# Performance work log

Measured on AMD Instinct MI355X. Metric: run time of the kernel, lower is better.

The kernel has to match this reference:

```python
import jax, jax.numpy as jnp
import numpy as np
import math

B, S, D, H = 2, 2048, 1024, 16
HD = D // H  # 64 head dim
DFF = 4 * D
ROPE_BASE = 10000.0
EPS = 1e-5


def setup_inputs() -> dict:
    key = jax.random.key(0)
    ks = jax.random.split(key, 16)
    w = lambda k, shp: jax.random.normal(k, shp, jnp.float32) * 0.02
    return {
        "x": jax.random.normal(ks[0], (B, S, D), jnp.float32),
        "Wq": w(ks[1], (D, D)), "bq": jnp.zeros((D,), jnp.float32),
        "Wk": w(ks[2], (D, D)), "bk": jnp.zeros((D,), jnp.float32),
        "Wv": w(ks[3], (D, D)), "bv": jnp.zeros((D,), jnp.float32),
        "Wo": w(ks[4], (D, D)), "bo": jnp.zeros((D,), jnp.float32),
        "W1": w(ks[5], (D, DFF)), "b1": jnp.zeros((DFF,), jnp.float32),
        "W2": w(ks[6], (DFF, D)), "b2": jnp.zeros((D,), jnp.float32),
        "g_pre": jnp.ones((D,), jnp.float32), "be_pre": jnp.zeros((D,), jnp.float32),
        "g_post": jnp.ones((D,), jnp.float32), "be_post": jnp.zeros((D,), jnp.float32),
    }


def _layernorm(x, g, b):
    mu = jnp.mean(x, axis=-1, keepdims=True)
    var = jnp.mean(jnp.square(x - mu), axis=-1, keepdims=True)
    return (x - mu) * jax.lax.rsqrt(var + EPS) * g + b


def _rope(q, k):
    # q,k: [B,H,S,HD]; standard rotary embedding on head dim
    half = HD // 2
    inv_freq = 1.0 / (ROPE_BASE ** (jnp.arange(0, HD, 2, dtype=jnp.float32) / HD))  # [half]
    pos = jnp.arange(S, dtype=jnp.float32)
    freqs = pos[:, None] * inv_freq[None, :]           # [S, half]
    emb = jnp.concatenate([freqs, freqs], axis=-1)      # [S, HD]
    cos = jnp.cos(emb)[None, None]                      # [1,1,S,HD]
    sin = jnp.sin(emb)[None, None]

    def rot_half(t):
        return jnp.concatenate([-t[..., half:], t[..., :half]], axis=-1)

    return q * cos + rot_half(q) * sin, k * cos + rot_half(k) * sin


def reference(x, Wq, bq, Wk, bk, Wv, bv, Wo, bo, W1, b1, W2, b2,
              g_pre, be_pre, g_post, be_post):
    residual = x
    xn = _layernorm(x, g_pre, be_pre)

    def split_heads(t):  # [B,S,D] -> [B,H,S,HD]
        return t.reshape(B, S, H, HD).transpose(0, 2, 1, 3)

    q = split_heads(xn @ Wq + bq)
    k = split_heads(xn @ Wk + bk)
    v = split_heads(xn @ Wv + bv)
    q, k = _rope(q, k)

    scores = jnp.einsum("bhqd,bhkd->bhqk", q, k) / math.sqrt(HD)
    attn = jax.nn.softmax(scores, axis=-1)
    # NOTE: original applies causal mask AFTER softmax with fill -1e9 (no renorm)
    causal = jnp.tril(jnp.ones((S, S), jnp.float32))
    attn = jnp.where(causal == 0, jnp.float32(-1e9), attn)

    out = jnp.einsum("bhqk,bhkd->bhqd", attn, v)        # [B,H,S,HD]
    out = out.transpose(0, 2, 1, 3).reshape(B, S, D)
    out = out @ Wo + bo
    x = residual + out

    residual = x
    xn = _layernorm(x, g_post, be_post)
    ff = jax.nn.relu(xn @ W1 + b1) @ W2 + b2
    return residual + ff
```

## Files before the change

kernel.cpp:

```cpp
#include <hip/hip_runtime.h>
#include <stdint.h>

#define B_ 2
#define S_ 2048
#define D_ 1024
#define H_ 16
#define HD_ 64
#define DFF_ 4096
#define M_ 4096
#define QKV_STR 3072

typedef float           f4_t  __attribute__((ext_vector_type(4)));
typedef unsigned int    ui4_t __attribute__((ext_vector_type(4)));
typedef unsigned int    ui2_t __attribute__((ext_vector_type(2)));
typedef unsigned short  us4_t __attribute__((ext_vector_type(4)));
typedef unsigned short  us8_t __attribute__((ext_vector_type(8)));
typedef __bf16          bf8_t __attribute__((ext_vector_type(8)));

__device__ __forceinline__ float b2f(unsigned short u) {
    union { unsigned int u; float f; } v; v.u = ((unsigned int)u) << 16; return v.f;
}
__device__ __forceinline__ unsigned short f2b(float f) {
    union { float f; unsigned int u; } v; v.f = f;
    unsigned int u = v.u + 0x7fffu + ((v.u >> 16) & 1u);
    return (unsigned short)(u >> 16);
}
__device__ __forceinline__ unsigned cvt_pk_bf16(float lo, float hi) {
    unsigned r;
    asm("v_cvt_pk_bf16_f32 %0, %1, %2" : "=v"(r) : "v"(lo), "v"(hi));
    return r;
}
__device__ __forceinline__ void gll16(const unsigned short* g, unsigned short* l) {
    __builtin_amdgcn_global_load_lds((const __attribute__((address_space(1))) unsigned int*)g,
                                     (__attribute__((address_space(3))) unsigned int*)l,
                                     16, 0, 0);
}

__global__ __launch_bounds__(256) void k_prep(const float* __restrict__ Wq, const float* __restrict__ Wk,
                                              const float* __restrict__ Wv, const float* __restrict__ Wo,
                                              const float* __restrict__ W1, const float* __restrict__ W2,
                                              const float* __restrict__ bq, const float* __restrict__ bk,
                                              const float* __restrict__ bv,
                                              unsigned short* __restrict__ WqkvT, unsigned short* __restrict__ WoT,
                                              unsigned short* __restrict__ W1T, unsigned short* __restrict__ W2T,
                                              float* __restrict__ bqkv, float* __restrict__ tab) {
    const int j = blockIdx.x;
    if (j < 12288) {
        const float* src; unsigned short* dst; int R, C, jj;
        if (j < 3072)      { const int r = j >> 10; src = r == 0 ? Wq : (r == 1 ? Wk : Wv);
                             dst = WqkvT + (size_t)r * 1024 * 1024; R = 1024; C = 1024; jj = j & 1023; }
        else if (j < 4096) { src = Wo; dst = WoT; R = 1024; C = 1024; jj = j - 3072; }
        else if (j < 8192) { src = W1; dst = W1T; R = 1024; C = 4096; jj = j - 4096; }
        else               { src = W2; dst = W2T; R = 4096; C = 1024; jj = j - 8192; }
        const int ntx = C >> 5;
        const int bc = (jj % ntx) * 32, br = (jj / ntx) * 32;
        __shared__ float tile[32][33];
        const int tx = threadIdx.x & 31, ty = threadIdx.x >> 5;
#pragma unroll
        for (int i = ty; i < 32; i += 8)
            tile[i][tx] = src[(size_t)(br + i) * C + bc + tx];
        __syncthreads();
#pragma unroll
        for (int i = ty; i < 32; i += 8)
            dst[(size_t)(bc + i) * R + br + tx] = f2b(tile[tx][i]);
    } else if (j < 12300) {
        const int t = (j - 12288) * 256 + threadIdx.x;
        if (t < 1024) bqkv[t] = bq[t];
        else if (t < 2048) bqkv[t] = bk[t - 1024];
        else if (t < 3072) bqkv[t] = bv[t - 2048];
    } else {
        const int base = (j - 12300) * 256 + threadIdx.x;
#pragma unroll
        for (int e = 0; e < 32; e++) {
            const int idx = base + e * 2048;
            const int s = idx >> 5, i = idx & 31;
            const float freq = exp2f(-(float)i * 0.4152410118609203f);
            float sn, cs;
            sincosf((float)s * freq, &sn, &cs);
            tab[s * 64 + i] = cs;
            tab[s * 64 + 32 + i] = sn;
        }
    }
}

__global__ __launch_bounds__(256) void k_layernorm(const float* __restrict__ x,
                                                   const float* __restrict__ g,
                                                   const float* __restrict__ be,
                                                   unsigned short* __restrict__ out) {
    const int row = blockIdx.x;
    const int t = threadIdx.x;
    const float* xr = x + (size_t)row * D_;
    f4_t v = *(const f4_t*)&xr[t * 4];
    float s = v[0] + v[1] + v[2] + v[3];
#pragma unroll
    for (int o = 32; o >= 1; o >>= 1) s += __shfl_down(s, o);
    __shared__ float red[4];
    const int w = t >> 6, lane = t & 63;
    if (lane == 0) red[w] = s;
    __syncthreads();
    const float mean = (red[0] + red[1] + red[2] + red[3]) * (1.f / D_);
    f4_t d;
#pragma unroll
    for (int c = 0; c < 4; c++) d[c] = v[c] - mean;
    float ss = d[0]*d[0] + d[1]*d[1] + d[2]*d[2] + d[3]*d[3];
#pragma unroll
    for (int o = 32; o >= 1; o >>= 1) ss += __shfl_down(ss, o);
    __syncthreads();
    if (lane == 0) red[w] = ss;
    __syncthreads();
    const float var = (red[0] + red[1] + red[2] + red[3]) * (1.f / D_);
    const float rstd = rsqrtf(var + 1e-5f);
    f4_t gv = *(const f4_t*)&g[t * 4];
    f4_t bv = *(const f4_t*)&be[t * 4];
    us4_t o4;
#pragma unroll
    for (int c = 0; c < 4; c++) o4[c] = f2b(d[c] * rstd * gv[c] + bv[c]);
    *(us4_t*)&out[(size_t)row * D_ + t * 4] = o4;
}

#define VMW(n) asm volatile("s_waitcnt vmcnt(" #n ")" ::: "memory")
#define BAR()  __builtin_amdgcn_s_barrier()

template<int RELU, int BF16OUT, int RESID, int ROPE, int SPLIT>
__global__ __launch_bounds__(256) void k_gemm_bt(const unsigned short* __restrict__ A,
                                                 const unsigned short* __restrict__ Bt,
                                                 const float* __restrict__ bias,
                                                 const float* __restrict__ resid,
                                                 void* __restrict__ Cout,
                                                 const float* __restrict__ tab,
                                                 int M, int N, int K, int ldk, int nbx) {
    __shared__ __align__(16) unsigned short As0[128 * 32];
    __shared__ __align__(16) unsigned short Bs0[128 * 32];
    __shared__ __align__(16) unsigned short As1[128 * 32];
    __shared__ __align__(16) unsigned short Bs1[128 * 32];
    const int tid = threadIdx.x;
    const int cpx = gridDim.x >> 3;
    int nid = (blockIdx.x & 7) * cpx + (blockIdx.x >> 3);
    int half = 0;
    if (SPLIT) { half = nid >> 8; nid &= 255; A += 2048 * half; Bt += 2048 * half; }
    const int m0 = (nid / nbx) * 128, n0 = (nid % nbx) * 128;
    const int w = tid >> 6, lane = tid & 63;
    const int wr = w >> 1, wc = w & 1;
    const int lr = lane & 15, lg = lane >> 4;

    f4_t acc[4][4] = {};

    const int r1 = tid >> 2, q1 = tid & 3;
    const unsigned short* pA1 = A + (size_t)(m0 + r1) * ldk + q1 * 8;
    const unsigned short* pA2 = pA1 + (size_t)64 * ldk;
    const unsigned short* pB1 = Bt + (size_t)(n0 + r1) * ldk + q1 * 8;
    const unsigned short* pB2 = pB1 + (size_t)64 * ldk;
    const int wofs = w * 512;

#define STAGE(AS, BS, kk) do {                 \
        gll16(pA1 + (kk), (AS) + wofs);        \
        gll16(pA2 + (kk), (AS) + 2048 + wofs); \
        gll16(pB1 + (kk), (BS) + wofs);        \
        gll16(pB2 + (kk), (BS) + 2048 + wofs); } while (0)

#define COMPUTE(AS, BS) do {                                                     \
        bf8_t af[4], bfr[4];                                                     \
        _Pragma("unroll")                                                        \
        for (int f = 0; f < 4; f++) {                                            \
            af[f]  = *(const bf8_t*)&(AS)[(wr * 64 + f * 16 + lr) * 32 + lg * 8];\
            bfr[f] = *(const bf8_t*)&(BS)[(wc * 64 + f * 16 + lr) * 32 + lg * 8];\
        }                                                                        \
        _Pragma("unroll")                                                        \
        for (int mf = 0; mf < 4; mf++)                                           \
            _Pragma("unroll")                                                    \
            for (int nf = 0; nf < 4; nf++)                                       \
                acc[mf][nf] = __builtin_amdgcn_mfma_f32_16x16x32_bf16(           \
                    af[mf], bfr[nf], acc[mf][nf], 0, 0, 0); } while (0)

    STAGE(As0, Bs0, 0);
    for (int k0 = 0; k0 + 64 < K; k0 += 64) {
        STAGE(As1, Bs1, k0 + 32);
        VMW(4); BAR();
        COMPUTE(As0, Bs0);
        BAR();
        STAGE(As0, Bs0, k0 + 64);
        VMW(4); BAR();
        COMPUTE(As1, Bs1);
        BAR();
    }
    STAGE(As1, Bs1, K - 32);
    VMW(4); BAR();
    COMPUTE(As0, Bs0);
    VMW(0); BAR();
    COMPUTE(As1, Bs1);
#undef STAGE
#undef COMPUTE

    if (SPLIT) {
        unsigned short* outp = (unsigned short*)Cout + (size_t)half * ((size_t)M * N);
#pragma unroll
        for (int mf = 0; mf < 4; mf++)
#pragma unroll
            for (int nf = 0; nf < 4; nf++) {
                const int n = n0 + wc * 64 + nf * 16 + lr;
#pragma unroll
                for (int j = 0; j < 4; j++) {
                    const int m = m0 + wr * 64 + mf * 16 + lg * 4 + j;
                    outp[(size_t)m * N + n] = f2b(acc[mf][nf][j]);
                }
            }
        return;
    }
    if (ROPE) {
#pragma unroll
        for (int mf = 0; mf < 4; mf++)
#pragma unroll
            for (int nf = 0; nf < 4; nf++) {
                const float bv = bias[n0 + wc * 64 + nf * 16 + lr];
#pragma unroll
                for (int j = 0; j < 4; j++) acc[mf][nf][j] += bv;
            }
        if (n0 < 2048) {
#pragma unroll
            for (int mf = 0; mf < 4; mf++)
#pragma unroll
                for (int j = 0; j < 4; j++) {
                    const int srow = (m0 + wr * 64 + mf * 16 + lg * 4 + j) & 2047;
                    const float* tr = tab + srow * 64;
#pragma unroll
                    for (int t = 0; t < 2; t++) {
                        const float cs = tr[t * 16 + lr];
                        const float sn = tr[32 + t * 16 + lr];
                        const float lo = acc[mf][t][j], hi = acc[mf][t + 2][j];
                        acc[mf][t][j]     = lo * cs - hi * sn;
                        acc[mf][t + 2][j] = hi * cs + lo * sn;
                    }
                }
        }
        unsigned short* outp = (unsigned short*)Cout;
#pragma unroll
        for (int mf = 0; mf < 4; mf++)
#pragma unroll
            for (int nf = 0; nf < 4; nf++) {
                const int n = n0 + wc * 64 + nf * 16 + lr;
#pragma unroll
                for (int j = 0; j < 4; j++) {
                    const int m = m0 + wr * 64 + mf * 16 + lg * 4 + j;
                    outp[(size_t)m * N + n] = f2b(acc[mf][nf][j]);
                }
            }
        return;
    }
#pragma unroll
    for (int mf = 0; mf < 4; mf++) {
#pragma unroll
        for (int nf = 0; nf < 4; nf++) {
            const int n = n0 + wc * 64 + nf * 16 + lr;
            const float bv = bias[n];
#pragma unroll
            for (int j = 0; j < 4; j++) {
                const int m = m0 + wr * 64 + mf * 16 + lg * 4 + j;
                float val = acc[mf][nf][j] + bv;
                if (RESID) val += resid[(size_t)m * N + n];
                if (RELU) val = fmaxf(val, 0.f);
                if (BF16OUT) ((unsigned short*)Cout)[(size_t)m * N + n] = f2b(val);
                else         ((float*)Cout)[(size_t)m * N + n] = val;
            }
        }
    }
}

template<int RELU, int BF16OUT, int RESID>
__global__ __launch_bounds__(256) void k_gemm64(const unsigned short* __restrict__ A,
                                                const unsigned short* __restrict__ Bt,
                                                const float* __restrict__ bias,
                                                const float* __restrict__ resid,
                                                void* __restrict__ Cout,
                                                int M, int N, int K, int ldk, int nbx) {
    __shared__ __align__(16) unsigned short As0[64 * 32];
    __shared__ __align__(16) unsigned short Bs0[128 * 32];
    __shared__ __align__(16) unsigned short As1[64 * 32];
    __shared__ __align__(16) unsigned short Bs1[128 * 32];
    const int tid = threadIdx.x;
    const int cpx = gridDim.x >> 3;
    const int nid = (blockIdx.x & 7) * cpx + (blockIdx.x >> 3);
    const int m0 = (nid / nbx) * 64, n0 = (nid % nbx) * 128;
    const int w = tid >> 6, lane = tid & 63;
    const int wr = w >> 1, wc = w & 1;
    const int lr = lane & 15, lg = lane >> 4;

    f4_t acc[2][4] = {};

    const int r1 = tid >> 2, q1 = tid & 3;
    const unsigned short* pA1 = A + (size_t)(m0 + r1) * ldk + q1 * 8;
    const unsigned short* pB1 = Bt + (size_t)(n0 + r1) * ldk + q1 * 8;
    const unsigned short* pB2 = pB1 + (size_t)64 * ldk;
    const int wofs = w * 512;

#define STAGE(AS, BS, kk) do {                 \
        gll16(pA1 + (kk), (AS) + wofs);        \
        gll16(pB1 + (kk), (BS) + wofs);        \
        gll16(pB2 + (kk), (BS) + 2048 + wofs); } while (0)

#define COMPUTE(AS, BS) do {                                                     \
        bf8_t af[2], bfr[4];                                                     \
        _Pragma("unroll")                                                        \
        for (int f = 0; f < 2; f++)                                              \
            af[f] = *(const bf8_t*)&(AS)[(wr * 32 + f * 16 + lr) * 32 + lg * 8]; \
        _Pragma("unroll")                                                        \
        for (int f = 0; f < 4; f++)                                              \
            bfr[f] = *(const bf8_t*)&(BS)[(wc * 64 + f * 16 + lr) * 32 + lg * 8];\
        _Pragma("unroll")                                                        \
        for (int mf = 0; mf < 2; mf++)                                           \
            _Pragma("unroll")                                                    \
            for (int nf = 0; nf < 4; nf++)                                       \
                acc[mf][nf] = __builtin_amdgcn_mfma_f32_16x16x32_bf16(           \
                    af[mf], bfr[nf], acc[mf][nf], 0, 0, 0); } while (0)

    STAGE(As0, Bs0, 0);
    for (int k0 = 0; k0 + 64 < K; k0 += 64) {
        STAGE(As1, Bs1, k0 + 32);
        VMW(3); BAR();
        COMPUTE(As0, Bs0);
        BAR();
        STAGE(As0, Bs0, k0 + 64);
        VMW(3); BAR();
        COMPUTE(As1, Bs1);
        BAR();
    }
    STAGE(As1, Bs1, K - 32);
    VMW(3); BAR();
    COMPUTE(As0, Bs0);
    VMW(0); BAR();
    COMPUTE(As1, Bs1);
#undef STAGE
#undef COMPUTE

#pragma unroll
    for (int mf = 0; mf < 2; mf++) {
#pragma unroll
        for (int nf = 0; nf < 4; nf++) {
            const int n = n0 + wc * 64 + nf * 16 + lr;
            const float bv = bias[n];
#pragma unroll
            for (int j = 0; j < 4; j++) {
                const int m = m0 + wr * 32 + mf * 16 + lg * 4 + j;
                float val = acc[mf][nf][j] + bv;
                if (RESID) val += resid[(size_t)m * N + n];
                if (RELU) val = fmaxf(val, 0.f);
                if (BF16OUT) ((unsigned short*)Cout)[(size_t)m * N + n] = f2b(val);
                else         ((float*)Cout)[(size_t)m * N + n] = val;
            }
        }
    }
}

__global__ __launch_bounds__(256) void k_comb(const unsigned short* __restrict__ p,
                                              const float* __restrict__ x2,
                                              const float* __restrict__ b2,
                                              float* __restrict__ out) {
    const size_t idx = ((size_t)blockIdx.x * 256 + threadIdx.x) * 8;
    us8_t a = *(const us8_t*)(p + idx);
    us8_t b = *(const us8_t*)(p + (size_t)M_ * D_ + idx);
    const int n = (int)(idx & (D_ - 1));
    f4_t x0 = *(const f4_t*)(x2 + idx), x1 = *(const f4_t*)(x2 + idx + 4);
    f4_t b0 = *(const f4_t*)(b2 + n),  b1 = *(const f4_t*)(b2 + n + 4);
    f4_t o0, o1;
#pragma unroll
    for (int c = 0; c < 4; c++) {
        o0[c] = x0[c] + b0[c] + b2f(a[c]) + b2f(b[c]);
        o1[c] = x1[c] + b1[c] + b2f(a[4 + c]) + b2f(b[4 + c]);
    }
    *(f4_t*)(out + idx) = o0;
    *(f4_t*)(out + idx + 4) = o1;
}

__global__ __launch_bounds__(256) void k_vchunksum(const unsigned short* __restrict__ V,
                                                   float* __restrict__ sums) {
    const int blk = blockIdx.x;
    const int bh = blk >> 5, c = blk & 31;
    const int b = bh >> 4, h = bh & 15;
    const int d = threadIdx.x & 63, r4 = threadIdx.x >> 6;
    const unsigned short* base = V + ((size_t)(b * S_ + c * 64 + r4 * 16)) * QKV_STR + h * HD_ + d;
    float s = 0.f;
#pragma unroll
    for (int r = 0; r < 16; r++) s += b2f(base[(size_t)r * QKV_STR]);
    __shared__ float red[4][64];
    red[r4][d] = s;
    __syncthreads();
    if (r4 == 0) sums[(size_t)blk * 64 + d] = red[0][d] + red[1][d] + red[2][d] + red[3][d];
}

__global__ __launch_bounds__(64) void k_vscan(const float* __restrict__ sums,
                                              float* __restrict__ pre) {
    const int bh = blockIdx.x, d = threadIdx.x;
    float cum = 0.f;
    for (int c = 0; c < 32; c++) {
        pre[((size_t)bh * 33 + c) * 64 + d] = cum;
        cum += sums[((size_t)bh * 32 + c) * 64 + d];
    }
    pre[((size_t)bh * 33 + 32) * 64 + d] = cum;
}

#define KS_STRIDE 72

__global__ __launch_bounds__(256) void k_attn_mfma(const unsigned short* __restrict__ QKV,
                                                   const float* __restrict__ vpre,
                                                   unsigned short* __restrict__ Out) {
    __shared__ __align__(16) unsigned short Ks[2][64 * KS_STRIDE];
    __shared__ __align__(16) unsigned short Vt[2][64 * 64];
    __shared__ __align__(16) unsigned short Ps[4][2][16 * KS_STRIDE];

    const int id = blockIdx.x;
    const int wg = (id & 7) * 64 + (id >> 3);
    const int qblk = 15 - (wg & 15);
    const int bh = wg >> 4;
    const int b = bh >> 4, h = bh & 15;
    const int q0 = qblk * 128;
    const int tid = threadIdx.x;
    const int wq = tid >> 6;
    const int lane = tid & 63;
    const int lr = lane & 15, lg = lane >> 4;

    const unsigned short* Qp = QKV;
    const unsigned short* Kp = QKV + 1024;
    const unsigned short* Vp = QKV + 2048;

    const int kcd = 2 * qblk + (wq >> 1);
    const int lastV = 2 * qblk + 1;
    int qb[2];
    qb[0] = (wq & 1) * 32 + lr;
    qb[1] = qb[0] + 16;

    bf8_t qfrag[2][2];
#pragma unroll
    for (int t = 0; t < 2; t++) {
        const float qs = 0.125f * 1.44269504f;
        const size_t qbase = ((size_t)(b * S_ + q0 + wq * 32 + t * 16 + lr)) * QKV_STR + h * HD_;
#pragma unroll
        for (int ks = 0; ks < 2; ks++) {
            us8_t raw = *(const us8_t*)(Qp + qbase + ks * 32 + lg * 8);
            ui4_t p;
#pragma unroll
            for (int e = 0; e < 4; e++)
                p[e] = cvt_pk_bf16(b2f(raw[e * 2]) * qs, b2f(raw[e * 2 + 1]) * qs);
            union { ui4_t u; bf8_t b; } c; c.u = p;
            qfrag[t][ks] = c.b;
        }
    }

    const int row0 = tid >> 3, g = tid & 7;
    const int row1 = row0 + 32;
    const int r7 = row0 & 7;
    const int wv = tid >> 6;
    const unsigned short* pK0 = Kp + ((size_t)(b * S_ + row0)) * QKV_STR + h * HD_ + g * 8;
    const unsigned short* pK1 = Kp + ((size_t)(b * S_ + row1)) * QKV_STR + h * HD_ + g * 8;
    const unsigned short* pV0 = Vp + ((size_t)(b * S_ + row0)) * QKV_STR + h * HD_ + g * 8;
    const unsigned short* pV1 = Vp + ((size_t)(b * S_ + row1)) * QKV_STR + h * HD_ + g * 8;
    const int sw0 = (wv ^ g) << 3;
    const int sw1 = ((wv + 4) ^ g) << 3;

    float l_run[2] = {0.f, 0.f};
    f4_t acc_o[2][4] = {};
    f4_t acc_pre[2][4] = {};

    ui4_t ck0 = *(const ui4_t*)pK0;
    ui4_t ck1 = *(const ui4_t*)pK1;
    ui4_t cv0 = *(const ui4_t*)pV0;
    ui4_t cv1 = *(const ui4_t*)pV1;
    *(ui4_t*)&Ks[0][row0 * KS_STRIDE + g * 8] = ck0;
    *(ui4_t*)&Ks[0][row1 * KS_STRIDE + g * 8] = ck1;
    {
        const unsigned short* v0 = (const unsigned short*)&cv0;
        const unsigned short* v1 = (const unsigned short*)&cv1;
#pragma unroll
        for (int e = 0; e < 8; e++) {
            const int d = g * 8 + e;
            Vt[0][d * 64 + sw0 + r7] = v0[e];
            Vt[0][d * 64 + sw1 + r7] = v1[e];
        }
    }
    {
        const size_t koff = (size_t)64 * QKV_STR;
        ck0 = *(const ui4_t*)(pK0 + koff);
        ck1 = *(const ui4_t*)(pK1 + koff);
        cv0 = *(const ui4_t*)(pV0 + koff);
        cv1 = *(const ui4_t*)(pV1 + koff);
    }
    __syncthreads();

#define VSLOT(dd, ks) ((((ks) * 4 + lg) ^ (((dd) * 2 + (lr >> 3)) & 7)) << 3)

    for (int kc = 0; kc < 32; kc++) {
        const int cur = kc & 1;
        const unsigned short* Kc = Ks[cur];
        const unsigned short* Vc = Vt[cur];

        f4_t s4[2][4] = {};
        __builtin_amdgcn_s_setprio(1);
#pragma unroll
        for (int ks = 0; ks < 2; ks++) {
#pragma unroll
            for (int kk = 0; kk < 4; kk++) {
                bf8_t kfr = *(const bf8_t*)&Kc[(kk * 16 + lr) * KS_STRIDE + ks * 32 + lg * 8];
                s4[0][kk] = __builtin_amdgcn_mfma_f32_16x16x32_bf16(kfr, qfrag[0][ks], s4[0][kk], 0, 0, 0);
                s4[1][kk] = __builtin_amdgcn_mfma_f32_16x16x32_bf16(kfr, qfrag[1][ks], s4[1][kk], 0, 0, 0);
            }
        }
        __builtin_amdgcn_s_setprio(0);

        if (kc < 31) {
            unsigned short* Kn = Ks[cur ^ 1];
            *(ui4_t*)&Kn[row0 * KS_STRIDE + g * 8] = ck0;
            *(ui4_t*)&Kn[row1 * KS_STRIDE + g * 8] = ck1;
            if (kc + 1 <= lastV) {
                unsigned short* Vn = Vt[cur ^ 1];
                const unsigned short* v0 = (const unsigned short*)&cv0;
                const unsigned short* v1 = (const unsigned short*)&cv1;
#pragma unroll
                for (int e = 0; e < 8; e++) {
                    const int d = g * 8 + e;
                    Vn[d * 64 + sw0 + r7] = v0[e];
                    Vn[d * 64 + sw1 + r7] = v1[e];
                }
            }
        }
        if (kc < 30) {
            const size_t koff = (size_t)(kc + 2) * 64 * QKV_STR;
            ck0 = *(const ui4_t*)(pK0 + koff);
            ck1 = *(const ui4_t*)(pK1 + koff);
            if (kc + 2 <= lastV) {
                cv0 = *(const ui4_t*)(pV0 + koff);
                cv1 = *(const ui4_t*)(pV1 + koff);
            }
        }

#pragma unroll
        for (int t = 0; t < 2; t++) {
            float cs = 0.f;
#pragma unroll
            for (int kk = 0; kk < 4; kk++)
#pragma unroll
                for (int j = 0; j < 4; j++) {
                    const float p = __builtin_amdgcn_exp2f(s4[t][kk][j]);
                    s4[t][kk][j] = p;
                    cs += p;
                }
            cs += __shfl_xor(cs, 16);
            cs += __shfl_xor(cs, 32);
            l_run[t] += cs;
        }

        if (kc <= kcd) {
#pragma unroll
            for (int t = 0; t < 2; t++) {
                unsigned short* Pw = Ps[wq][t];
#pragma unroll
                for (int kk = 0; kk < 4; kk++) {
                    const int kb = kk * 16 + lg * 4;
                    ui2_t wd;
                    if (kc == kcd) {
                        wd[0] = cvt_pk_bf16(kb + 0 <= qb[t] ? s4[t][kk][0] : 0.f,
                                            kb + 1 <= qb[t] ? s4[t][kk][1] : 0.f);
                        wd[1] = cvt_pk_bf16(kb + 2 <= qb[t] ? s4[t][kk][2] : 0.f,
                                            kb + 3 <= qb[t] ? s4[t][kk][3] : 0.f);
                    } else {
                        wd[0] = cvt_pk_bf16(s4[t][kk][0], s4[t][kk][1]);
                        wd[1] = cvt_pk_bf16(s4[t][kk][2], s4[t][kk][3]);
                    }
                    *(ui2_t*)&Pw[lr * KS_STRIDE + kk * 16 + lg * 4] = wd;
                }
            }
            __builtin_amdgcn_s_setprio(1);
#pragma unroll
            for (int ks = 0; ks < 2; ks++) {
                bf8_t pf0 = *(const bf8_t*)&Ps[wq][0][lr * KS_STRIDE + ks * 32 + lg * 8];
                bf8_t pf1 = *(const bf8_t*)&Ps[wq][1][lr * KS_STRIDE + ks * 32 + lg * 8];
#pragma unroll
                for (int dd = 0; dd < 4; dd++) {
                    bf8_t vf = *(const bf8_t*)&Vc[(dd * 16 + lr) * 64 + VSLOT(dd, ks)];
                    acc_o[0][dd] = __builtin_amdgcn_mfma_f32_16x16x32_bf16(vf, pf0, acc_o[0][dd], 0, 0, 0);
                    acc_o[1][dd] = __builtin_amdgcn_mfma_f32_16x16x32_bf16(vf, pf1, acc_o[1][dd], 0, 0, 0);
                }
            }
            __builtin_amdgcn_s_setprio(0);

            if (kc == kcd) {
#pragma unroll
                for (int t = 0; t < 2; t++) {
                    unsigned short* Pw = Ps[wq][t];
#pragma unroll
                    for (int kk = 0; kk < 4; kk++) {
                        const int kb = kk * 16 + lg * 4;
                        ui2_t wd;
                        wd[0] = (kb + 0 <= qb[t] ? 0x3f80u : 0u) | ((kb + 1 <= qb[t] ? 0x3f80u : 0u) << 16);
                        wd[1] = (kb + 2 <= qb[t] ? 0x3f80u : 0u) | ((kb + 3 <= qb[t] ? 0x3f80u : 0u) << 16);
                        *(ui2_t*)&Pw[lr * KS_STRIDE + kk * 16 + lg * 4] = wd;
                    }
                }
#pragma unroll
                for (int ks = 0; ks < 2; ks++) {
                    bf8_t pf0 = *(const bf8_t*)&Ps[wq][0][lr * KS_STRIDE + ks * 32 + lg * 8];
                    bf8_t pf1 = *(const bf8_t*)&Ps[wq][1][lr * KS_STRIDE + ks * 32 + lg * 8];
#pragma unroll
                    for (int dd = 0; dd < 4; dd++) {
                        bf8_t vf = *(const bf8_t*)&Vc[(dd * 16 + lr) * 64 + VSLOT(dd, ks)];
                        acc_pre[0][dd] = __builtin_amdgcn_mfma_f32_16x16x32_bf16(vf, pf0, acc_pre[0][dd], 0, 0, 0);
                        acc_pre[1][dd] = __builtin_amdgcn_mfma_f32_16x16x32_bf16(vf, pf1, acc_pre[1][dd], 0, 0, 0);
                    }
                }
            }
        }
        __syncthreads();
    }
#undef VSLOT

    const float* Cq = vpre + ((size_t)bh * 33 + kcd) * 64;
    const float* Ct = vpre + ((size_t)bh * 33 + 32) * 64;
#pragma unroll
    for (int t = 0; t < 2; t++) {
        const float inv_l = 1.f / l_run[t];
        const size_t obase = ((size_t)(b * S_ + q0 + wq * 32 + t * 16 + lr)) * D_ + h * HD_;
#pragma unroll
        for (int dd = 0; dd < 4; dd++) {
            const f4_t tq4 = *(const f4_t*)&Cq[dd * 16 + lg * 4];
            const f4_t tt4 = *(const f4_t*)&Ct[dd * 16 + lg * 4];
            float v[4];
#pragma unroll
            for (int j = 0; j < 4; j++)
                v[j] = acc_o[t][dd][j] * inv_l - 1e9f * (tt4[j] - tq4[j] - acc_pre[t][dd][j]);
            ui2_t wd;
            wd[0] = cvt_pk_bf16(v[0], v[1]);
            wd[1] = cvt_pk_bf16(v[2], v[3]);
            *(ui2_t*)&Out[obase + dd * 16 + lg * 4] = wd;
        }
    }
}

extern "C" void kernel_launch(void* const* d_in, const int* in_sizes, int n_in,
                              void* d_out, int out_size, void* d_ws, size_t ws_size,
                              hipStream_t stream) {
    const float* x     = (const float*)d_in[0];
    const float* Wq    = (const float*)d_in[1];  const float* bq = (const float*)d_in[2];
    const float* Wk    = (const float*)d_in[3];  const float* bk = (const float*)d_in[4];
    const float* Wv    = (const float*)d_in[5];  const float* bv = (const float*)d_in[6];
    const float* Wo    = (const float*)d_in[7];  const float* bo = (const float*)d_in[8];
    const float* W1    = (const float*)d_in[9];  const float* b1 = (const float*)d_in[10];
    const float* W2    = (const float*)d_in[11]; const float* b2 = (const float*)d_in[12];
    const float* gpre  = (const float*)d_in[13]; const float* bepre  = (const float*)d_in[14];
    const float* gpost = (const float*)d_in[15]; const float* bepost = (const float*)d_in[16];

    char* ws = (char*)d_ws;
    const size_t MB = 1024 * 1024;
    unsigned short* psplit = (unsigned short*)(ws + 0 * MB);
    unsigned short* WqkvT = (unsigned short*)(ws + 0 * MB);
    unsigned short* WoT   = (unsigned short*)(ws + 6 * MB);
    unsigned short* W1T   = (unsigned short*)(ws + 8 * MB);
    unsigned short* W2T   = (unsigned short*)(ws + 16 * MB);
    unsigned short* xn    = (unsigned short*)(ws + 24 * MB);
    unsigned short* x2n   = (unsigned short*)(ws + 24 * MB);
    unsigned short* QKV   = (unsigned short*)(ws + 32 * MB);
    unsigned short* h1    = (unsigned short*)(ws + 32 * MB);
    unsigned short* att   = (unsigned short*)(ws + 56 * MB);
    float*          x2    = (float*)(ws + 64 * MB);
    float*          bqkv  = (float*)(ws + 80 * MB);
    float*          vpre  = (float*)(ws + 80 * MB + 16384);
    float*          tab   = (float*)(ws + 80 * MB + 512 * 1024);
    float*          vsum  = (float*)(ws + 81 * MB);

    k_prep<<<12308, 256, 0, stream>>>(Wq, Wk, Wv, Wo, W1, W2, bq, bk, bv,
                                      WqkvT, WoT, W1T, W2T, bqkv, tab);

    k_layernorm<<<M_, 256, 0, stream>>>(x, gpre, bepre, xn);

    k_gemm_bt<0, 1, 0, 1, 0><<<768, 256, 0, stream>>>(xn, WqkvT, bqkv, nullptr, QKV, tab,
                                                      M_, QKV_STR, D_, D_, 24);

    k_vchunksum<<<1024, 256, 0, stream>>>(QKV + 2048, vsum);
    k_vscan<<<32, 64, 0, stream>>>(vsum, vpre);

    k_attn_mfma<<<512, 256, 0, stream>>>(QKV, vpre, att);

    k_gemm64<0, 0, 1><<<512, 256, 0, stream>>>(att, WoT, bo, x, x2, M_, D_, D_, D_, 8);

    k_layernorm<<<M_, 256, 0, stream>>>(x2, gpost, bepost, x2n);

    k_gemm_bt<1, 1, 0, 0, 0><<<1024, 256, 0, stream>>>(x2n, W1T, b1, nullptr, h1, nullptr,
                                                       M_, DFF_, D_, D_, 32);

    k_gemm_bt<0, 1, 0, 0, 1><<<512, 256, 0, stream>>>(h1, W2T, nullptr, nullptr, psplit, nullptr,
                                                      M_, D_, 2048, DFF_, 8);
    k_comb<<<2048, 256, 0, stream>>>(psplit, x2, b2, (float*)d_out);
}
```

Before: 249.7 us.

## Fuse V chunk sums into QKV GEMM epilogue and widen FFN1 GEMM tile

The QKV projection epilogue now reduces each 64-row chunk of the V columns across lanes and writes the per-chunk column sums directly, so the separate V chunk-sum kernel and its re-read of V are removed. Those sums are taken from fp32 accumulators rather than bf16-rounded values, which slightly changes the numerics. The first FFN GEMM moves to a new 128x256-tile kernel to get more reuse of A per block, at the cost of more registers and LDS per block and fewer blocks in the grid.

New measurement: 260.6 us. +4.4%, slower.

```diff
diff --git a/kernel.cpp b/kernel.cpp
--- a/kernel.cpp
+++ b/kernel.cpp
@@ -128,6 +128,7 @@
                                                  const float* __restrict__ resid,
                                                  void* __restrict__ Cout,
                                                  const float* __restrict__ tab,
+                                                 float* __restrict__ vsout,
                                                  int M, int N, int K, int ldk, int nbx) {
     __shared__ __align__(16) unsigned short As0[128 * 32];
     __shared__ __align__(16) unsigned short Bs0[128 * 32];
@@ -215,7 +216,30 @@
 #pragma unroll
                 for (int j = 0; j < 4; j++) acc[mf][nf][j] += bv;
             }
-        if (n0 < 2048) {
+        const int ncol0 = n0 + wc * 64;
+        if (ncol0 >= 2048) {
+            float csum[4];
+#pragma unroll
+            for (int nf = 0; nf < 4; nf++) {
+                float s = 0.f;
+#pragma unroll
+                for (int mf = 0; mf < 4; mf++)
+#pragma unroll
+                    for (int j = 0; j < 4; j++) s += acc[mf][nf][j];
+                s += __shfl_xor(s, 16);
+                s += __shfl_xor(s, 32);
+                csum[nf] = s;
+            }
+            if (lg == 0) {
+                const int mrow = m0 + wr * 64;
+                const int bb = mrow >> 11, c = (mrow & 2047) >> 6;
+                const int hh = (ncol0 - 2048) >> 6;
+                const int bh = bb * 16 + hh;
+#pragma unroll
+                for (int nf = 0; nf < 4; nf++)
+                    vsout[((size_t)(bh * 32 + c)) * 64 + nf * 16 + lr] = csum[nf];
+            }
+        } else {
 #pragma unroll
             for (int mf = 0; mf < 4; mf++)
 #pragma unroll
@@ -260,6 +284,94 @@
                 if (RELU) val = fmaxf(val, 0.f);
                 if (BF16OUT) ((unsigned short*)Cout)[(size_t)m * N + n] = f2b(val);
                 else         ((float*)Cout)[(size_t)m * N + n] = val;
+            }
+        }
+    }
+}
+
+template<int RELU>
+__global__ __launch_bounds__(256) void k_gemm_wide(const unsigned short* __restrict__ A,
+                                                   const unsigned short* __restrict__ Bt,
+                                                   const float* __restrict__ bias,
+                                                   unsigned short* __restrict__ Cout,
+                                                   int M, int N, int K, int nbx) {
+    __shared__ __align__(16) unsigned short As0[128 * 32];
+    __shared__ __align__(16) unsigned short Bs0[256 * 32];
+    __shared__ __align__(16) unsigned short As1[128 * 32];
+    __shared__ __align__(16) unsigned short Bs1[256 * 32];
+    const int tid = threadIdx.x;
+    const int cpx = gridDim.x >> 3;
+    const int nid = (blockIdx.x & 7) * cpx + (blockIdx.x >> 3);
+    const int m0 = (nid / nbx) * 128, n0 = (nid % nbx) * 256;
+    const int w = tid >> 6, lane = tid & 63;
+    const int wr = w >> 1, wc = w & 1;
+    const int lr = lane & 15, lg = lane >> 4;
+
+    f4_t acc[4][8] = {};
+
+    const int r1 = tid >> 2, q1 = tid & 3;
+    const unsigned short* pA1 = A + (size_t)(m0 + r1) * K + q1 * 8;
+    const unsigned short* pA2 = pA1 + (size_t)64 * K;
+    const unsigned short* pB1 = Bt + (size_t)(n0 + r1) * K + q1 * 8;
+    const unsigned short* pB2 = pB1 + (size_t)64 * K;
+    const unsigned short* pB3 = pB1 + (size_t)128 * K;
+    const unsigned short* pB4 = pB1 + (size_t)192 * K;
+    const int wofs = w * 512;
+
+#define STAGE(AS, BS, kk) do {                 \
+        gll16(pA1 + (kk), (AS) + wofs);        \
+        gll16(pA2 + (kk), (AS) + 2048 + wofs); \
+        gll16(pB1 + (kk), (BS) + wofs);        \
+        gll16(pB2 + (kk), (BS) + 2048 + wofs); \
+        gll16(pB3 + (kk), (BS) + 4096 + wofs); \
+        gll16(pB4 + (kk), (BS) + 6144 + wofs); } while (0)
+
+#define COMPUTE(AS, BS) do {                                                      \
+        bf8_t af[4], bfr[8];                                                      \
+        _Pragma("unroll")                                                         \
+        for (int f = 0; f < 4; f++)                                               \
+            af[f] = *(const bf8_t*)&(AS)[(wr * 64 + f * 16 + lr) * 32 + lg * 8];  \
+        _Pragma("unroll")                                                         \
+        for (int f = 0; f < 8; f++)                                               \
+            bfr[f] = *(const bf8_t*)&(BS)[(wc * 128 + f * 16 + lr) * 32 + lg * 8];\
+        _Pragma("unroll")                                                         \
+        for (int mf = 0; mf < 4; mf++)                                            \
+            _Pragma("unroll")                                                     \
+            for (int nf = 0; nf < 8; nf++)                                        \
+                acc[mf][nf] = __builtin_amdgcn_mfma_f32_16x16x32_bf16(            \
+                    af[mf], bfr[nf], acc[mf][nf], 0, 0, 0); } while (0)
+
+    STAGE(As0, Bs0, 0);
+    for (int k0 = 0; k0 + 64 < K; k0 += 64) {
+        STAGE(As1, Bs1, k0 + 32);
+        VMW(6); BAR();
+        COMPUTE(As0, Bs0);
+        BAR();
+        STAGE(As0, Bs0, k0 + 64);
+        VMW(6); BAR();
+        COMPUTE(As1, Bs1);
+        BAR();
+    }
+    STAGE(As1, Bs1, K - 32);
+    VMW(6); BAR();
+    COMPUTE(As0, Bs0);
+    VMW(0); BAR();
+    COMPUTE(As1, Bs1);
+#undef STAGE
+#undef COMPUTE
+
+#pragma unroll
+    for (int mf = 0; mf < 4; mf++) {
+#pragma unroll
+        for (int nf = 0; nf < 8; nf++) {
+            const int n = n0 + wc * 128 + nf * 16 + lr;
+            const float bv = bias[n];
+#pragma unroll
+            for (int j = 0; j < 4; j++) {
+                const int m = m0 + wr * 64 + mf * 16 + lg * 4 + j;
+                float val = acc[mf][nf][j] + bv;
+                if (RELU) val = fmaxf(val, 0.f);
+                Cout[(size_t)m * N + n] = f2b(val);
             }
         }
     }
@@ -370,22 +482,6 @@
     *(f4_t*)(out + idx + 4) = o1;
 }
 
-__global__ __launch_bounds__(256) void k_vchunksum(const unsigned short* __restrict__ V,
-                                                   float* __restrict__ sums) {
-    const int blk = blockIdx.x;
-    const int bh = blk >> 5, c = blk & 31;
-    const int b = bh >> 4, h = bh & 15;
-    const int d = threadIdx.x & 63, r4 = threadIdx.x >> 6;
-    const unsigned short* base = V + ((size_t)(b * S_ + c * 64 + r4 * 16)) * QKV_STR + h * HD_ + d;
-    float s = 0.f;
-#pragma unroll
-    for (int r = 0; r < 16; r++) s += b2f(base[(size_t)r * QKV_STR]);
-    __shared__ float red[4][64];
-    red[r4][d] = s;
-    __syncthreads();
-    if (r4 == 0) sums[(size_t)blk * 64 + d] = red[0][d] + red[1][d] + red[2][d] + red[3][d];
-}
-
 __global__ __launch_bounds__(64) void k_vscan(const float* __restrict__ sums,
                                               float* __restrict__ pre) {
     const int bh = blockIdx.x, d = threadIdx.x;
@@ -668,10 +764,9 @@
 
     k_layernorm<<<M_, 256, 0, stream>>>(x, gpre, bepre, xn);
 
-    k_gemm_bt<0, 1, 0, 1, 0><<<768, 256, 0, stream>>>(xn, WqkvT, bqkv, nullptr, QKV, tab,
+    k_gemm_bt<0, 1, 0, 1, 0><<<768, 256, 0, stream>>>(xn, WqkvT, bqkv, nullptr, QKV, tab, vsum,
                                                       M_, QKV_STR, D_, D_, 24);
 
-    k_vchunksum<<<1024, 256, 0, stream>>>(QKV + 2048, vsum);
     k_vscan<<<32, 64, 0, stream>>>(vsum, vpre);
 
     k_attn_mfma<<<512, 256, 0, stream>>>(QKV, vpre, att);
@@ -680,10 +775,9 @@
 
     k_layernorm<<<M_, 256, 0, stream>>>(x2, gpost, bepost, x2n);
 
-    k_gemm_bt<1, 1, 0, 0, 0><<<1024, 256, 0, stream>>>(x2n, W1T, b1, nullptr, h1, nullptr,
-                                                       M_, DFF_, D_, D_, 32);
-
-    k_gemm_bt<0, 1, 0, 0, 1><<<512, 256, 0, stream>>>(h1, W2T, nullptr, nullptr, psplit, nullptr,
+    k_gemm_wide<1><<<512, 256, 0, stream>>>(x2n, W1T, b1, h1, M_, DFF_, D_, 16);
+
+    k_gemm_bt<0, 1, 0, 0, 1><<<512, 256, 0, stream>>>(h1, W2T, nullptr, nullptr, psplit, nullptr, nullptr,
                                                       M_, D_, 2048, DFF_, 8);
     k_comb<<<2048, 256, 0, stream>>>(psplit, x2, b2, (float*)d_out);
 }
```

## Pair mirrored 64-row query blocks per workgroup to balance causal attention work

Applied to the files above, without the earlier changes.

Each workgroup now processes two 64-row query tiles, qA and 31-qA, instead of one contiguous 128-row tile. This evens out causal work across workgroups. The P·V MFMAs for tile A are skipped once the key chunk passes its diagonal, and the diagonal correction is done per tile. The goal is to remove tail imbalance, where blocks with late query positions run much longer than early ones. The cost is extra branching and a hidden part of the loop, QK and softmax, that may still compute scores for tile A past its diagonal.

Result: no change. 247.5 us (-0.9%).

```diff
diff --git a/kernel.cpp b/kernel.cpp
--- a/kernel.cpp
+++ b/kernel.cpp
@@ -408,10 +408,10 @@
 
     const int id = blockIdx.x;
     const int wg = (id & 7) * 64 + (id >> 3);
-    const int qblk = 15 - (wg & 15);
+    const int qA = wg & 15;
+    const int qB = 31 - qA;
     const int bh = wg >> 4;
     const int b = bh >> 4, h = bh & 15;
-    const int q0 = qblk * 128;
     const int tid = threadIdx.x;
     const int wq = tid >> 6;
     const int lane = tid & 63;
@@ -421,17 +421,16 @@
     const unsigned short* Kp = QKV + 1024;
     const unsigned short* Vp = QKV + 2048;
 
-    const int kcd = 2 * qblk + (wq >> 1);
-    const int lastV = 2 * qblk + 1;
-    int qb[2];
-    qb[0] = (wq & 1) * 32 + lr;
-    qb[1] = qb[0] + 16;
+    const int kcdt[2] = {qA, qB};
+    const int lastV = qB;
+    const int qb = wq * 16 + lr;
+    const int q0t[2] = {qA * 64, qB * 64};
 
     bf8_t qfrag[2][2];
 #pragma unroll
     for (int t = 0; t < 2; t++) {
         const float qs = 0.125f * 1.44269504f;
-        const size_t qbase = ((size_t)(b * S_ + q0 + wq * 32 + t * 16 + lr)) * QKV_STR + h * HD_;
+        const size_t qbase = ((size_t)(b * S_ + q0t[t] + wq * 16 + lr)) * QKV_STR + h * HD_;
 #pragma unroll
         for (int ks = 0; ks < 2; ks++) {
             us8_t raw = *(const us8_t*)(Qp + qbase + ks * 32 + lg * 8);
@@ -546,62 +545,76 @@
             l_run[t] += cs;
         }
 
-        if (kc <= kcd) {
-#pragma unroll
-            for (int t = 0; t < 2; t++) {
-                unsigned short* Pw = Ps[wq][t];
+        if (kc <= qB) {
+            const bool doA = (kc <= qA);
+#pragma unroll
+            for (int kk = 0; kk < 4; kk++) {
+                const int kb = kk * 16 + lg * 4;
+                ui2_t wd;
+                if (kc == qB) {
+                    wd[0] = cvt_pk_bf16(kb + 0 <= qb ? s4[1][kk][0] : 0.f,
+                                        kb + 1 <= qb ? s4[1][kk][1] : 0.f);
+                    wd[1] = cvt_pk_bf16(kb + 2 <= qb ? s4[1][kk][2] : 0.f,
+                                        kb + 3 <= qb ? s4[1][kk][3] : 0.f);
+                } else {
+                    wd[0] = cvt_pk_bf16(s4[1][kk][0], s4[1][kk][1]);
+                    wd[1] = cvt_pk_bf16(s4[1][kk][2], s4[1][kk][3]);
+                }
+                *(ui2_t*)&Ps[wq][1][lr * KS_STRIDE + kk * 16 + lg * 4] = wd;
+            }
+            if (doA) {
 #pragma unroll
                 for (int kk = 0; kk < 4; kk++) {
                     const int kb = kk * 16 + lg * 4;
                     ui2_t wd;
-                    if (kc == kcd) {
-                        wd[0] = cvt_pk_bf16(kb + 0 <= qb[t] ? s4[t][kk][0] : 0.f,
-                                            kb + 1 <= qb[t] ? s4[t][kk][1] : 0.f);
-                        wd[1] = cvt_pk_bf16(kb + 2 <= qb[t] ? s4[t][kk][2] : 0.f,
-                                            kb + 3 <= qb[t] ? s4[t][kk][3] : 0.f);
+                    if (kc == qA) {
+                        wd[0] = cvt_pk_bf16(kb + 0 <= qb ? s4[0][kk][0] : 0.f,
+                                            kb + 1 <= qb ? s4[0][kk][1] : 0.f);
+                        wd[1] = cvt_pk_bf16(kb + 2 <= qb ? s4[0][kk][2] : 0.f,
+                                            kb + 3 <= qb ? s4[0][kk][3] : 0.f);
                     } else {
-                        wd[0] = cvt_pk_bf16(s4[t][kk][0], s4[t][kk][1]);
-                        wd[1] = cvt_pk_bf16(s4[t][kk][2], s4[t][kk][3]);
+                        wd[0] = cvt_pk_bf16(s4[0][kk][0], s4[0][kk][1]);
+                        wd[1] = cvt_pk_bf16(s4[0][kk][2], s4[0][kk][3]);
                     }
-                    *(ui2_t*)&Pw[lr * KS_STRIDE + kk * 16 + lg * 4] = wd;
+                    *(ui2_t*)&Ps[wq][0][lr * KS_STRIDE + kk * 16 + lg * 4] = wd;
                 }
             }
             __builtin_amdgcn_s_setprio(1);
 #pragma unroll
             for (int ks = 0; ks < 2; ks++) {
-                bf8_t pf0 = *(const bf8_t*)&Ps[wq][0][lr * KS_STRIDE + ks * 32 + lg * 8];
                 bf8_t pf1 = *(const bf8_t*)&Ps[wq][1][lr * KS_STRIDE + ks * 32 + lg * 8];
+                bf8_t pf0;
+                if (doA) pf0 = *(const bf8_t*)&Ps[wq][0][lr * KS_STRIDE + ks * 32 + lg * 8];
 #pragma unroll
                 for (int dd = 0; dd < 4; dd++) {
                     bf8_t vf = *(const bf8_t*)&Vc[(dd * 16 + lr) * 64 + VSLOT(dd, ks)];
-                    acc_o[0][dd] = __builtin_amdgcn_mfma_f32_16x16x32_bf16(vf, pf0, acc_o[0][dd], 0, 0, 0);
                     acc_o[1][dd] = __builtin_amdgcn_mfma_f32_16x16x32_bf16(vf, pf1, acc_o[1][dd], 0, 0, 0);
+                    if (doA)
+                        acc_o[0][dd] = __builtin_amdgcn_mfma_f32_16x16x32_bf16(vf, pf0, acc_o[0][dd], 0, 0, 0);
                 }
             }
             __builtin_amdgcn_s_setprio(0);
 
-            if (kc == kcd) {
-#pragma unroll
-                for (int t = 0; t < 2; t++) {
+#pragma unroll
+            for (int t = 0; t < 2; t++) {
+                if (kc == kcdt[t]) {
                     unsigned short* Pw = Ps[wq][t];
 #pragma unroll
                     for (int kk = 0; kk < 4; kk++) {
                         const int kb = kk * 16 + lg * 4;
                         ui2_t wd;
-                        wd[0] = (kb + 0 <= qb[t] ? 0x3f80u : 0u) | ((kb + 1 <= qb[t] ? 0x3f80u : 0u) << 16);
-                        wd[1] = (kb + 2 <= qb[t] ? 0x3f80u : 0u) | ((kb + 3 <= qb[t] ? 0x3f80u : 0u) << 16);
+                        wd[0] = (kb + 0 <= qb ? 0x3f80u : 0u) | ((kb + 1 <= qb ? 0x3f80u : 0u) << 16);
+                        wd[1] = (kb + 2 <= qb ? 0x3f80u : 0u) | ((kb + 3 <= qb ? 0x3f80u : 0u) << 16);
                         *(ui2_t*)&Pw[lr * KS_STRIDE + kk * 16 + lg * 4] = wd;
                     }
-                }
-#pragma unroll
-                for (int ks = 0; ks < 2; ks++) {
-                    bf8_t pf0 = *(const bf8_t*)&Ps[wq][0][lr * KS_STRIDE + ks * 32 + lg * 8];
-                    bf8_t pf1 = *(const bf8_t*)&Ps[wq][1][lr * KS_STRIDE + ks * 32 + lg * 8];
-#pragma unroll
-                    for (int dd = 0; dd < 4; dd++) {
-                        bf8_t vf = *(const bf8_t*)&Vc[(dd * 16 + lr) * 64 + VSLOT(dd, ks)];
-                        acc_pre[0][dd] = __builtin_amdgcn_mfma_f32_16x16x32_bf16(vf, pf0, acc_pre[0][dd], 0, 0, 0);
-                        acc_pre[1][dd] = __builtin_amdgcn_mfma_f32_16x16x32_bf16(vf, pf1, acc_pre[1][dd], 0, 0, 0);
+#pragma unroll
+                    for (int ks = 0; ks < 2; ks++) {
+                        bf8_t pf = *(const bf8_t*)&Pw[lr * KS_STRIDE + ks * 32 + lg * 8];
+#pragma unroll
+                        for (int dd = 0; dd < 4; dd++) {
+                            bf8_t vf = *(const bf8_t*)&Vc[(dd * 16 + lr) * 64 + VSLOT(dd, ks)];
+                            acc_pre[t][dd] = __builtin_amdgcn_mfma_f32_16x16x32_bf16(vf, pf, acc_pre[t][dd], 0, 0, 0);
+                        }
                     }
                 }
             }
@@ -610,12 +623,12 @@
     }
 #undef VSLOT
 
-    const float* Cq = vpre + ((size_t)bh * 33 + kcd) * 64;
     const float* Ct = vpre + ((size_t)bh * 33 + 32) * 64;
 #pragma unroll
     for (int t = 0; t < 2; t++) {
+        const float* Cq = vpre + ((size_t)bh * 33 + kcdt[t]) * 64;
         const float inv_l = 1.f / l_run[t];
-        const size_t obase = ((size_t)(b * S_ + q0 + wq * 32 + t * 16 + lr)) * D_ + h * HD_;
+        const size_t obase = ((size_t)(b * S_ + q0t[t] + wq * 16 + lr)) * D_ + h * HD_;
 #pragma unroll
         for (int dd = 0; dd < 4; dd++) {
             const f4_t tq4 = *(const f4_t*)&Cq[dd * 16 + lg * 4];
```
